# Kernel tuning notes

Hardware: AMD Instinct MI355X
Metric: run time of the kernel (lower is better)

Reference implementation:

```python
import jax, jax.numpy as jnp
import numpy as np
import math

DIM = 2048
N_HEADS = 16
HEAD_DIM = DIM // N_HEADS  # 128
SEQ = 2048
EPS = 1e-5
NEG = -1e9


def get_slopes(n):
    # n is a power of 2 here (16)
    start = 2.0 ** (-2.0 ** (-(math.log2(n) - 3)))
    return [start * start ** i for i in range(n)]


def setup_inputs() -> dict:
    key = jax.random.key(0)
    ks = jax.random.split(key, 6)
    x = jax.random.normal(ks[0], (1, SEQ, DIM), dtype=jnp.float32)
    # causal additive mask (large negative above diagonal)
    causal = jnp.tril(jnp.ones((SEQ, SEQ), dtype=bool))
    mask = jnp.where(causal, 0.0, NEG).astype(jnp.float32)[None, None]
    scale_w = 0.02
    wq = jax.random.normal(ks[1], (DIM, DIM), dtype=jnp.float32) * scale_w  # [in, out]
    wk = jax.random.normal(ks[2], (DIM, DIM), dtype=jnp.float32) * scale_w
    wv = jax.random.normal(ks[3], (DIM, DIM), dtype=jnp.float32) * scale_w
    wo = jax.random.normal(ks[4], (DIM, DIM), dtype=jnp.float32) * scale_w
    # AttentionPrior params: shape_init=1, scale_init='slope' (stored as log), loc_init=0
    shape = jnp.ones((1, N_HEADS, 1, 1), dtype=jnp.float32)
    scale = jnp.log(jnp.asarray(get_slopes(N_HEADS), dtype=jnp.float32)).reshape(1, N_HEADS, 1, 1)
    loc = jnp.zeros((1, N_HEADS, 1, 1), dtype=jnp.float32)
    return {"x": x, "mask": mask, "wq": wq, "wk": wk, "wv": wv, "wo": wo,
            "shape": shape, "scale": scale, "loc": loc, "start_pos": 0}


def _prior_bias(shape, scale, loc, seqlen, start_pos):
    q_pos = jnp.arange(seqlen, dtype=jnp.float32) + start_pos
    k_pos = jnp.arange(seqlen + start_pos, dtype=jnp.float32)
    dist = (k_pos[None, :] - q_pos[:, None])[None, None]  # [1,1,S,K]
    loc_t = jnp.exp(loc) - jnp.exp(-loc)
    z = (dist - loc_t) * jnp.exp(scale)  # [1,H,S,K]
    return -(jnp.abs(z) + EPS) ** shape


def reference(x, mask, wq, wk, wv, wo, shape, scale, loc, start_pos):
    bsz, seqlen, _ = x.shape
    q = (x @ wq).reshape(bsz, seqlen, N_HEADS, HEAD_DIM)
    k = (x @ wk).reshape(bsz, seqlen, N_HEADS, HEAD_DIM)
    v = (x @ wv).reshape(bsz, seqlen, N_HEADS, HEAD_DIM)
    # start_pos=0 prefill: cache slice == current keys/values
    scores = jnp.einsum('bqhd,bkhd->bhqk', q, k) / math.sqrt(HEAD_DIM)
    scores = scores + _prior_bias(shape, scale, loc, seqlen, start_pos)
    scores = scores + mask
    probs = jax.nn.softmax(scores.astype(jnp.float32), axis=-1).astype(q.dtype)
    out = jnp.einsum('bhqk,bkhd->bqhd', probs, v).reshape(bsz, seqlen, DIM)
    return out @ wo
```

## Files before the change

### kernel.cpp

```cpp
#include <hip/hip_runtime.h>
#include <hip/hip_bf16.h>
#include <stdint.h>


typedef unsigned short u16;
typedef unsigned int u32;

using bf16x8 = __attribute__((ext_vector_type(8))) __bf16;
using f32x4  = __attribute__((ext_vector_type(4))) float;

__device__ __forceinline__ u16 f2bf(float f) {
  union { float f; u32 u; } v; v.f = f;
  u32 r = (v.u + 0x7FFFu + ((v.u >> 16) & 1u)) >> 16;
  return (u16)r;
}

__device__ __forceinline__ u16 f2bfn(float f) {
  union { __bf16 b; u16 u; } c; c.b = (__bf16)f; return c.u;
}

__device__ __forceinline__ float bf2f(u16 h) {
  union { u32 u; float f; } v; v.u = ((u32)h) << 16; return v.f;
}

__device__ __forceinline__ void gload16(const void* g, void* l) {
  __builtin_amdgcn_global_load_lds((const __attribute__((address_space(1))) void*)g,
                                   (__attribute__((address_space(3))) void*)l, 16, 0, 0);
}

__device__ __forceinline__ int cumch128(int qt) {
  if (qt < 4)  return qt;
  if (qt < 8)  return 4 + 2 * (qt - 4);
  if (qt < 12) return 12 + 3 * (qt - 8);
  return 24 + 4 * (qt - 12);
}

__global__ __launch_bounds__(256) void prep(const float* __restrict__ x, const float* __restrict__ wq,
                                            const float* __restrict__ wk, const float* __restrict__ wv,
                                            const float* __restrict__ wo,
                                            u16* __restrict__ xb, u16* __restrict__ wqkt,
                                            u16* __restrict__ wvt, u16* __restrict__ wot) {
  __shared__ float tile[32][33];
  const int z = blockIdx.z;
  const int t = threadIdx.x;
  if (z == 4) {
    int i = ((blockIdx.y * 64 + blockIdx.x) * 256 + t);
    float4 v = ((const float4*)x)[i];
    ushort4 o;
    o.x = f2bf(v.x); o.y = f2bf(v.y); o.z = f2bf(v.z); o.w = f2bf(v.w);
    ((ushort4*)xb)[i] = o;
    return;
  }
  const float* src = (z == 0) ? wq : (z == 1) ? wk : (z == 2) ? wv : wo;
  u16* dst = (z == 0) ? wqkt : (z == 1) ? (wqkt + 2048 * 2048) : (z == 2) ? wvt : wot;
  const int c0 = blockIdx.x * 32, r0 = blockIdx.y * 32;
  const int ci = t & 31, rj = t >> 5;
#pragma unroll
  for (int j = 0; j < 4; ++j)
    tile[rj + j * 8][ci] = src[(size_t)(r0 + rj + j * 8) * 2048 + c0 + ci];
  __syncthreads();
#pragma unroll
  for (int j = 0; j < 4; ++j) {
    int rr = rj + j * 8;
    dst[(size_t)(c0 + rr) * 2048 + r0 + ci] = f2bf(tile[ci][rr]);
  }
}

__global__ __launch_bounds__(256) void gemm_qkv(const u16* __restrict__ xb, const u16* __restrict__ wqkt,
                                                const u16* __restrict__ wvt,
                                                u16* __restrict__ qkc, u16* __restrict__ vtc) {
  __shared__ u16 lds[16384];
  int bid = blockIdx.x;
  const u16 *A, *Bt;
  u16* C;
  int N, bn, bm, scl_cols;
  if (bid < 512) { A = xb;  Bt = wqkt; C = qkc; N = 4096; bn = bid & 31; bm = bid >> 5; scl_cols = 2048; }
  else { bid -= 512; A = wvt; Bt = xb; C = vtc; N = 2048; bn = bid & 15; bm = bid >> 4; scl_cols = 0; }
  const int K = 2048;

  const int t = threadIdx.x;
  const int w = t >> 6, l = t & 63;
  const int wm = w >> 1, wn = w & 1;
  const int lrow = l & 15, lgrp = l >> 4;

  f32x4 acc[4][4] = {};

  for (int k0 = 0; k0 < K; k0 += 64) {
    if (k0) __syncthreads();
#pragma unroll
    for (int p = 0; p < 4; ++p) {
      int i = (p * 4 + w) * 64 + l;
      int r = i >> 3, u = i & 7;
      const u16* src = A + (size_t)(bm * 128 + r) * K + k0 + ((u ^ (r & 7)) << 3);
      gload16(src, (char*)lds + (p * 4 + w) * 1024);
    }
#pragma unroll
    for (int p = 0; p < 4; ++p) {
      int i = (p * 4 + w) * 64 + l;
      int r = i >> 3, u = i & 7;
      const u16* src = Bt + (size_t)(bn * 128 + r) * K + k0 + ((u ^ (r & 7)) << 3);
      gload16(src, (char*)lds + 16384 + (p * 4 + w) * 1024);
    }
    __syncthreads();

#pragma unroll
    for (int kc = 0; kc < 2; ++kc) {
      bf16x8 af[4], bfr[4];
#pragma unroll
      for (int mt = 0; mt < 4; ++mt) {
        int rho = wm * 64 + mt * 16 + lrow;
        int un = (kc * 4 + lgrp) ^ (rho & 7);
        af[mt] = *(const bf16x8*)((const char*)lds + rho * 128 + un * 16);
      }
#pragma unroll
      for (int nt = 0; nt < 4; ++nt) {
        int rho = wn * 64 + nt * 16 + lrow;
        int un = (kc * 4 + lgrp) ^ (rho & 7);
        bfr[nt] = *(const bf16x8*)((const char*)lds + 16384 + rho * 128 + un * 16);
      }
#pragma unroll
      for (int mt = 0; mt < 4; ++mt)
#pragma unroll
        for (int nt = 0; nt < 4; ++nt)
          acc[mt][nt] = __builtin_amdgcn_mfma_f32_16x16x32_bf16(af[mt], bfr[nt], acc[mt][nt], 0, 0, 0);
    }
  }

  const int row0 = bm * 128 + wm * 64;
  const int col0 = bn * 128 + wn * 64;
#pragma unroll
  for (int mt = 0; mt < 4; ++mt)
#pragma unroll
    for (int nt = 0; nt < 4; ++nt) {
      int col = col0 + nt * 16 + lrow;
      float s = (col < scl_cols) ? 0.08838834764831843f : 1.0f;
#pragma unroll
      for (int r = 0; r < 4; ++r) {
        int row = row0 + mt * 16 + lgrp * 4 + r;
        C[(size_t)row * N + col] = f2bf(acc[mt][nt][r] * s);
      }
    }
}

__global__ __launch_bounds__(256) void gemm_out(const u16* __restrict__ A, const u16* __restrict__ Bt,
                                                float* __restrict__ out) {
  __shared__ u16 lds[12288];
  const int bn = blockIdx.x, bm = blockIdx.y;
  const int K = 2048;

  const int t = threadIdx.x;
  const int w = t >> 6, l = t & 63;
  const int wm = w >> 1, wn = w & 1;
  const int lrow = l & 15, lgrp = l >> 4;

  f32x4 acc[4][2] = {};

  for (int k0 = 0; k0 < K; k0 += 64) {
    if (k0) __syncthreads();
#pragma unroll
    for (int p = 0; p < 4; ++p) {
      int i = p * 256 + t;
      int r = i >> 3, u = i & 7;
      const u16* src = A + (size_t)(bm * 128 + r) * K + k0 + ((u ^ (r & 7)) << 3);
      gload16(src, (char*)lds + i * 16);
    }
#pragma unroll
    for (int p = 0; p < 2; ++p) {
      int i = p * 256 + t;
      int r = i >> 3, u = i & 7;
      const u16* src = Bt + (size_t)(bn * 64 + r) * K + k0 + ((u ^ (r & 7)) << 3);
      gload16(src, (char*)lds + 16384 + i * 16);
    }
    __syncthreads();

#pragma unroll
    for (int kc = 0; kc < 2; ++kc) {
      bf16x8 af[4], bfr[2];
#pragma unroll
      for (int mt = 0; mt < 4; ++mt) {
        int rho = wm * 64 + mt * 16 + lrow;
        int un = (kc * 4 + lgrp) ^ (rho & 7);
        af[mt] = *(const bf16x8*)((const char*)lds + rho * 128 + un * 16);
      }
#pragma unroll
      for (int nt = 0; nt < 2; ++nt) {
        int rho = wn * 32 + nt * 16 + lrow;
        int un = (kc * 4 + lgrp) ^ (rho & 7);
        bfr[nt] = *(const bf16x8*)((const char*)lds + 16384 + rho * 128 + un * 16);
      }
#pragma unroll
      for (int mt = 0; mt < 4; ++mt)
#pragma unroll
        for (int nt = 0; nt < 2; ++nt)
          acc[mt][nt] = __builtin_amdgcn_mfma_f32_16x16x32_bf16(af[mt], bfr[nt], acc[mt][nt], 0, 0, 0);
    }
  }

  const int row0 = bm * 128 + wm * 64;
  const int col0 = bn * 64 + wn * 32;
#pragma unroll
  for (int mt = 0; mt < 4; ++mt)
#pragma unroll
    for (int nt = 0; nt < 2; ++nt) {
      int col = col0 + nt * 16 + lrow;
#pragma unroll
      for (int r = 0; r < 4; ++r) {
        int row = row0 + mt * 16 + lgrp * 4 + r;
        out[(size_t)row * 2048 + col] = acc[mt][nt][r];
      }
    }
}

__global__ __launch_bounds__(256) void attn_part(const u16* __restrict__ QK, const u16* __restrict__ Vt,
                                                 u16* __restrict__ Opart, float* __restrict__ Lpart,
                                                 const float* __restrict__ g_shape,
                                                 const float* __restrict__ g_scale,
                                                 const float* __restrict__ g_loc,
                                                 const int* __restrict__ g_sp) {
  __shared__ u16 k_lds[2][4096];
  __shared__ u16 v_lds[2][4096];
  __shared__ u16 p_lds[4][1280];

  const int raw = blockIdx.x;
  const int bid = (raw & 7) * 80 + (raw >> 3);
  const int h = bid / 40;
  const int rem = bid - h * 40;
  int qt, ch;
  if (rem < 4)       { qt = rem;                 ch = 0; }
  else if (rem < 12) { int r2 = rem - 4;  qt = 4  + (r2 >> 1); ch = r2 & 1; }
  else if (rem < 24) { int r3 = rem - 12; qt = 8  + r3 / 3;    ch = r3 - 3 * (r3 / 3); }
  else               { int r4 = rem - 24; qt = 12 + (r4 >> 2); ch = r4 & 3; }
  const int pid = bid;

  const int t = threadIdx.x, w = t >> 6, l = t & 63;
  const int lrow = l & 15, lgrp = l >> 4;

  const float sh = g_shape[h];
  const float es = __expf(g_scale[h]);
  const float lcv = g_loc[h];
  const float loc_t = __expf(lcv) - __expf(-lcv);
  const int sp = g_sp[0];
  const bool shape1 = (sh == 1.0f);

  const int qwave = qt * 128 + w * 32;

  bf16x8 qf[2][4];
#pragma unroll
  for (int mt = 0; mt < 2; ++mt) {
    const u16* qp = QK + (size_t)(qwave + mt * 16 + lrow) * 4096 + h * 128 + lgrp * 8;
#pragma unroll
    for (int kc = 0; kc < 4; ++kc) qf[mt][kc] = *(const bf16x8*)(qp + kc * 32);
  }

  f32x4 o[2][8] = {};
  float lr[2][4] = {};

  const int kstart = ch * 16;
  const int kend = min(kstart + 16, 4 * qt + 4);

#define STAGE_TILE(buf, kt_) do {                                                        \
    const int kv0s = (kt_) * 32;                                                         \
    _Pragma("unroll")                                                                    \
    for (int p = 0; p < 2; ++p) {                                                        \
      int i = p * 256 + t;                                                               \
      int r = i >> 4, u = i & 15;                                                        \
      const u16* src = QK + (size_t)(kv0s + r) * 4096 + 2048 + h * 128 + ((u ^ (r & 7)) << 3); \
      gload16(src, (char*)k_lds[buf] + i * 16);                                          \
    }                                                                                    \
    _Pragma("unroll")                                                                    \
    for (int p = 0; p < 2; ++p) {                                                        \
      int i = p * 256 + t;                                                               \
      int r = i >> 2, u = i & 3;                                                         \
      const u16* src = Vt + (size_t)(h * 128 + r) * 2048 + kv0s + ((u ^ ((r >> 2) & 3)) << 3); \
      gload16(src, (char*)v_lds[buf] + i * 16);                                          \
    }                                                                                    \
  } while (0)

  STAGE_TILE(0, kstart);
  __syncthreads();

  for (int kt = kstart; kt < kend; ++kt) {
    const int cur = (kt - kstart) & 1;
    if (kt + 1 < kend) STAGE_TILE(cur ^ 1, kt + 1);
    const int kv0 = kt * 32;

    f32x4 s4[2][2];
#pragma unroll
    for (int mt = 0; mt < 2; ++mt)
#pragma unroll
      for (int nc = 0; nc < 2; ++nc) s4[mt][nc] = f32x4{-11.0f, -11.0f, -11.0f, -11.0f};
#pragma unroll
    for (int kc = 0; kc < 4; ++kc) {
#pragma unroll
      for (int nc = 0; nc < 2; ++nc) {
        int rho = nc * 16 + lrow;
        int un = (kc * 4 + lgrp) ^ (rho & 7);
        bf16x8 bk = *(const bf16x8*)((const char*)k_lds[cur] + rho * 256 + un * 16);
        s4[0][nc] = __builtin_amdgcn_mfma_f32_16x16x32_bf16(qf[0][kc], bk, s4[0][nc], 0, 0, 0);
        s4[1][nc] = __builtin_amdgcn_mfma_f32_16x16x32_bf16(qf[1][kc], bk, s4[1][nc], 0, 0, 0);
      }
    }

    const bool need_mask = (kv0 + 31 > qwave + sp);
    if (shape1 && !need_mask) {
#pragma unroll
      for (int mt = 0; mt < 2; ++mt)
#pragma unroll
        for (int r = 0; r < 4; ++r) {
          const float fb = (float)(kv0 + lrow - (qwave + mt * 16 + lgrp * 4 + r) - sp) - loc_t;
#pragma unroll
          for (int nc = 0; nc < 2; ++nc) {
            float u = fb + (float)(nc * 16);
            float p = __expf(fmaf(-es, fabsf(u), s4[mt][nc][r]));
            lr[mt][r] += p;
            p_lds[w][(mt * 16 + lgrp * 4 + r) * 40 + nc * 16 + lrow] = f2bfn(p);
          }
        }
    } else if (shape1) {
#pragma unroll
      for (int mt = 0; mt < 2; ++mt)
#pragma unroll
        for (int r = 0; r < 4; ++r) {
          const float fb = (float)(kv0 + lrow - (qwave + mt * 16 + lgrp * 4 + r) - sp) - loc_t;
#pragma unroll
          for (int nc = 0; nc < 2; ++nc) {
            float u = fb + (float)(nc * 16);
            float p = __expf(fmaf(-es, fabsf(u), s4[mt][nc][r]));
            p = (u + loc_t > 0.0f) ? 0.0f : p;
            lr[mt][r] += p;
            p_lds[w][(mt * 16 + lgrp * 4 + r) * 40 + nc * 16 + lrow] = f2bfn(p);
          }
        }
    } else {
#pragma unroll
      for (int mt = 0; mt < 2; ++mt)
#pragma unroll
        for (int r = 0; r < 4; ++r) {
          const float fb = (float)(kv0 + lrow - (qwave + mt * 16 + lgrp * 4 + r) - sp) - loc_t;
#pragma unroll
          for (int nc = 0; nc < 2; ++nc) {
            float u = fb + (float)(nc * 16);
            float az = fmaf(es, fabsf(u), 1e-5f);
            float p = __expf(s4[mt][nc][r] - __powf(az, sh));
            p = (u + loc_t > 0.0f) ? 0.0f : p;
            lr[mt][r] += p;
            p_lds[w][(mt * 16 + lgrp * 4 + r) * 40 + nc * 16 + lrow] = f2bfn(p);
          }
        }
    }

    {
      bf16x8 pa0 = *(const bf16x8*)((const char*)p_lds[w] + lrow * 80 + lgrp * 16);
      bf16x8 pa1 = *(const bf16x8*)((const char*)p_lds[w] + (16 + lrow) * 80 + lgrp * 16);
#pragma unroll
      for (int dc = 0; dc < 8; ++dc) {
        int rho = dc * 16 + lrow;
        int un = lgrp ^ ((rho >> 2) & 3);
        bf16x8 bv = *(const bf16x8*)((const char*)v_lds[cur] + rho * 64 + un * 16);
        o[0][dc] = __builtin_amdgcn_mfma_f32_16x16x32_bf16(pa0, bv, o[0][dc], 0, 0, 0);
        o[1][dc] = __builtin_amdgcn_mfma_f32_16x16x32_bf16(pa1, bv, o[1][dc], 0, 0, 0);
      }
    }

    __syncthreads();
  }
#undef STAGE_TILE

#pragma unroll
  for (int mt = 0; mt < 2; ++mt)
#pragma unroll
    for (int r = 0; r < 4; ++r)
#pragma unroll
      for (int msk = 1; msk <= 8; msk <<= 1) lr[mt][r] += __shfl_xor(lr[mt][r], msk);

  u16* ob = Opart + (size_t)pid * 16384;
#pragma unroll
  for (int mt = 0; mt < 2; ++mt)
#pragma unroll
    for (int dc = 0; dc < 8; ++dc)
#pragma unroll
      for (int r = 0; r < 4; ++r) {
        int row = w * 32 + mt * 16 + lgrp * 4 + r;
        ob[(size_t)row * 128 + dc * 16 + lrow] = f2bfn(o[mt][dc][r]);
      }
  if (lrow == 0) {
#pragma unroll
    for (int mt = 0; mt < 2; ++mt)
#pragma unroll
      for (int r = 0; r < 4; ++r) {
        int row = w * 32 + mt * 16 + lgrp * 4 + r;
        Lpart[(size_t)pid * 128 + row] = lr[mt][r];
      }
  }
}

__global__ __launch_bounds__(256) void attn_merge(const u16* __restrict__ Opart,
                                                  const float* __restrict__ Lpart,
                                                  u16* __restrict__ AO) {
  const int bid = blockIdx.x;
  const int qt = bid & 15, h = bid >> 4;
  const int nch = (qt >> 2) + 1;
  const int base = h * 40 + cumch128(qt);
  const int t = threadIdx.x;
  const int row = t >> 1;
  const int dseg = (t & 1) << 6;

  float acc[64] = {};
  float lstar = 0.0f;
#pragma unroll
  for (int i = 0; i < 4; ++i) {
    if (i < nch) {
      lstar += Lpart[(size_t)(base + i) * 128 + row];
      const ushort4* op = (const ushort4*)(Opart + (size_t)(base + i) * 16384 + row * 128 + dseg);
#pragma unroll
      for (int j = 0; j < 16; ++j) {
        ushort4 v = op[j];
        acc[j * 4 + 0] += bf2f(v.x); acc[j * 4 + 1] += bf2f(v.y);
        acc[j * 4 + 2] += bf2f(v.z); acc[j * 4 + 3] += bf2f(v.w);
      }
    }
  }
  const float inv = 1.0f / lstar;
  const int q_abs = qt * 128 + row;
  u16* dst = AO + (size_t)q_abs * 2048 + h * 128 + dseg;
#pragma unroll
  for (int j = 0; j < 16; ++j) {
    ushort4 ov;
    ov.x = f2bf(acc[j * 4 + 0] * inv); ov.y = f2bf(acc[j * 4 + 1] * inv);
    ov.z = f2bf(acc[j * 4 + 2] * inv); ov.w = f2bf(acc[j * 4 + 3] * inv);
    *(ushort4*)(dst + j * 4) = ov;
  }
}

extern "C" void kernel_launch(void* const* d_in, const int* in_sizes, int n_in,
                              void* d_out, int out_size, void* d_ws, size_t ws_size,
                              hipStream_t stream) {
  const float* x   = (const float*)d_in[0];
  const float* wq  = (const float*)d_in[2];
  const float* wk  = (const float*)d_in[3];
  const float* wv  = (const float*)d_in[4];
  const float* wo  = (const float*)d_in[5];
  const float* shp = (const float*)d_in[6];
  const float* scl = (const float*)d_in[7];
  const float* loc = (const float*)d_in[8];
  const int*   sp  = (const int*)d_in[9];

  char* ws = (char*)d_ws;
  u16*   xb    = (u16*)(ws);
  u16*   wqkt  = (u16*)(ws + (size_t)( 8u << 20));
  u16*   wvt   = (u16*)(ws + (size_t)(24u << 20));
  u16*   opart = (u16*)(ws);
  u16*   wot   = (u16*)(ws + (size_t)(40u << 20));
  u16*   qk    = (u16*)(ws + (size_t)(48u << 20));
  u16*   vt    = (u16*)(ws + (size_t)(64u << 20));
  u16*   ao    = (u16*)(ws + (size_t)(72u << 20));
  float* lpart = (float*)(ws + (size_t)(80u << 20));

  hipLaunchKernelGGL(prep, dim3(64, 64, 5), dim3(256), 0, stream,
                     x, wq, wk, wv, wo, xb, wqkt, wvt, wot);
  hipLaunchKernelGGL(gemm_qkv, dim3(768), dim3(256), 0, stream, xb, wqkt, wvt, qk, vt);
  hipLaunchKernelGGL(attn_part, dim3(640), dim3(256), 0, stream,
                     qk, vt, opart, lpart, shp, scl, loc, sp);
  hipLaunchKernelGGL(attn_merge, dim3(256), dim3(256), 0, stream, opart, lpart, ao);
  hipLaunchKernelGGL(gemm_out, dim3(32, 16), dim3(256), 0, stream, ao, wot, (float*)d_out);
}
```

Before: 167.8 us.

## Move Wo transpose into QKV GEMM launch and split merge across more blocks

The Wo conversion and transpose is taken out of the prep kernel and done by 64 extra blocks appended to the QKV GEMM grid, each handling 64 tiles. This lets the Wo work overlap with the GEMM tail instead of sitting in prep's critical path. Separately, attn_merge now uses twice as many blocks, each covering half the head dimension, so there are fewer registers per thread and more parallelism. The risk is that the extra transpose blocks get scheduled last and lengthen the GEMM kernel's tail.

Result: slower. 186.0 us (+10.8%).

```diff
diff --git a/kernel.cpp b/kernel.cpp
--- a/kernel.cpp
+++ b/kernel.cpp
@@ -37,13 +37,12 @@
 
 __global__ __launch_bounds__(256) void prep(const float* __restrict__ x, const float* __restrict__ wq,
                                             const float* __restrict__ wk, const float* __restrict__ wv,
-                                            const float* __restrict__ wo,
                                             u16* __restrict__ xb, u16* __restrict__ wqkt,
-                                            u16* __restrict__ wvt, u16* __restrict__ wot) {
+                                            u16* __restrict__ wvt) {
   __shared__ float tile[32][33];
   const int z = blockIdx.z;
   const int t = threadIdx.x;
-  if (z == 4) {
+  if (z == 3) {
     int i = ((blockIdx.y * 64 + blockIdx.x) * 256 + t);
     float4 v = ((const float4*)x)[i];
     ushort4 o;
@@ -51,8 +50,8 @@
     ((ushort4*)xb)[i] = o;
     return;
   }
-  const float* src = (z == 0) ? wq : (z == 1) ? wk : (z == 2) ? wv : wo;
-  u16* dst = (z == 0) ? wqkt : (z == 1) ? (wqkt + 2048 * 2048) : (z == 2) ? wvt : wot;
+  const float* src = (z == 0) ? wq : (z == 1) ? wk : wv;
+  u16* dst = (z == 0) ? wqkt : (z == 1) ? (wqkt + 2048 * 2048) : wvt;
   const int c0 = blockIdx.x * 32, r0 = blockIdx.y * 32;
   const int ci = t & 31, rj = t >> 5;
 #pragma unroll
@@ -68,9 +67,32 @@
 
 __global__ __launch_bounds__(256) void gemm_qkv(const u16* __restrict__ xb, const u16* __restrict__ wqkt,
                                                 const u16* __restrict__ wvt,
+                                                const float* __restrict__ wo, u16* __restrict__ wot,
                                                 u16* __restrict__ qkc, u16* __restrict__ vtc) {
   __shared__ u16 lds[16384];
   int bid = blockIdx.x;
+  const int t = threadIdx.x;
+
+  if (bid >= 768) {
+    float (*tile)[33] = (float(*)[33])lds;
+    const int ci = t & 31, rj = t >> 5;
+    for (int j = 0; j < 64; ++j) {
+      int tidx = (bid - 768) * 64 + j;
+      int c0 = (tidx & 63) * 32, r0 = (tidx >> 6) * 32;
+      if (j) __syncthreads();
+#pragma unroll
+      for (int jj = 0; jj < 4; ++jj)
+        tile[rj + jj * 8][ci] = wo[(size_t)(r0 + rj + jj * 8) * 2048 + c0 + ci];
+      __syncthreads();
+#pragma unroll
+      for (int jj = 0; jj < 4; ++jj) {
+        int rr = rj + jj * 8;
+        wot[(size_t)(c0 + rr) * 2048 + r0 + ci] = f2bf(tile[ci][rr]);
+      }
+    }
+    return;
+  }
+
   const u16 *A, *Bt;
   u16* C;
   int N, bn, bm, scl_cols;
@@ -78,7 +100,6 @@
   else { bid -= 512; A = wvt; Bt = xb; C = vtc; N = 2048; bn = bid & 15; bm = bid >> 4; scl_cols = 0; }
   const int K = 2048;
 
-  const int t = threadIdx.x;
   const int w = t >> 6, l = t & 63;
   const int wm = w >> 1, wn = w & 1;
   const int lrow = l & 15, lgrp = l >> 4;
@@ -398,14 +419,15 @@
                                                   const float* __restrict__ Lpart,
                                                   u16* __restrict__ AO) {
   const int bid = blockIdx.x;
-  const int qt = bid & 15, h = bid >> 4;
+  const int half = bid & 1;
+  const int qt = (bid >> 1) & 15, h = bid >> 5;
   const int nch = (qt >> 2) + 1;
   const int base = h * 40 + cumch128(qt);
   const int t = threadIdx.x;
   const int row = t >> 1;
-  const int dseg = (t & 1) << 6;
-
-  float acc[64] = {};
+  const int dseg = ((t & 1) << 5) + (half << 6);
+
+  float acc[32] = {};
   float lstar = 0.0f;
 #pragma unroll
   for (int i = 0; i < 4; ++i) {
@@ -413,7 +435,7 @@
       lstar += Lpart[(size_t)(base + i) * 128 + row];
       const ushort4* op = (const ushort4*)(Opart + (size_t)(base + i) * 16384 + row * 128 + dseg);
 #pragma unroll
-      for (int j = 0; j < 16; ++j) {
+      for (int j = 0; j < 8; ++j) {
         ushort4 v = op[j];
         acc[j * 4 + 0] += bf2f(v.x); acc[j * 4 + 1] += bf2f(v.y);
         acc[j * 4 + 2] += bf2f(v.z); acc[j * 4 + 3] += bf2f(v.w);
@@ -424,7 +446,7 @@
   const int q_abs = qt * 128 + row;
   u16* dst = AO + (size_t)q_abs * 2048 + h * 128 + dseg;
 #pragma unroll
-  for (int j = 0; j < 16; ++j) {
+  for (int j = 0; j < 8; ++j) {
     ushort4 ov;
     ov.x = f2bf(acc[j * 4 + 0] * inv); ov.y = f2bf(acc[j * 4 + 1] * inv);
     ov.z = f2bf(acc[j * 4 + 2] * inv); ov.w = f2bf(acc[j * 4 + 3] * inv);
@@ -456,11 +478,12 @@
   u16*   ao    = (u16*)(ws + (size_t)(72u << 20));
   float* lpart = (float*)(ws + (size_t)(80u << 20));
 
-  hipLaunchKernelGGL(prep, dim3(64, 64, 5), dim3(256), 0, stream,
-                     x, wq, wk, wv, wo, xb, wqkt, wvt, wot);
-  hipLaunchKernelGGL(gemm_qkv, dim3(768), dim3(256), 0, stream, xb, wqkt, wvt, qk, vt);
+  hipLaunchKernelGGL(prep, dim3(64, 64, 4), dim3(256), 0, stream,
+                     x, wq, wk, wv, xb, wqkt, wvt);
+  hipLaunchKernelGGL(gemm_qkv, dim3(832), dim3(256), 0, stream,
+                     xb, wqkt, wvt, wo, wot, qk, vt);
   hipLaunchKernelGGL(attn_part, dim3(640), dim3(256), 0, stream,
                      qk, vt, opart, lpart, shp, scl, loc, sp);
-  hipLaunchKernelGGL(attn_merge, dim3(256), dim3(256), 0, stream, opart, lpart, ao);
+  hipLaunchKernelGGL(attn_merge, dim3(512), dim3(256), 0, stream, opart, lpart, ao);
   hipLaunchKernelGGL(gemm_out, dim3(32, 16), dim3(256), 0, stream, ao, wot, (float*)d_out);
 }
```
